# Kernel tuning notes

Measured on AMD Instinct MI355X. Metric: run time of the kernel, lower is better.

## Reference

```python
import jax, jax.numpy as jnp
import numpy as np
import math

D_MODEL = 1024
N_HEADS = 16
D_K = 64
CHUNK_LEN = 64


def setup_inputs() -> dict:
    key = jax.random.key(0)
    ks = jax.random.split(key, 12)
    hd = N_HEADS * D_K
    s = 0.02
    return {
        'h': jax.random.normal(ks[0], (4, 2048, D_MODEL), jnp.float32),
        'e': jax.random.normal(ks[1], (4, 32, 2, 128, D_MODEL), jnp.float32),
        'Wq': jax.random.normal(ks[2], (D_MODEL, hd), jnp.float32) * s,
        'bq': jnp.zeros((hd,), jnp.float32),
        'Wk': jax.random.normal(ks[3], (D_MODEL, hd), jnp.float32) * s,
        'bk': jnp.zeros((hd,), jnp.float32),
        'Wv': jax.random.normal(ks[4], (D_MODEL, hd), jnp.float32) * s,
        'bv': jnp.zeros((hd,), jnp.float32),
        'Wo': jax.random.normal(ks[5], (hd, D_MODEL), jnp.float32) * s,
        'bo': jnp.zeros((D_MODEL,), jnp.float32),
        'gamma': jnp.ones((D_MODEL,), jnp.float32),
        'beta': jnp.zeros((D_MODEL,), jnp.float32),
    }


def reference(h, e, Wq, bq, Wk, bk, Wv, bv, Wo, bo, gamma, beta):
    b, chunks, neighbors, nlen, d_model = e.shape
    seq_len = h.shape[1]
    scale = 1.0 / math.sqrt(D_K)
    h_res = h
    # shift so chunk i attends to neighbors retrieved for chunk i
    hh = h[:, CHUNK_LEN - 1:]
    # layer norm
    mu = jnp.mean(hh, axis=-1, keepdims=True)
    var = jnp.mean(jnp.square(hh - mu), axis=-1, keepdims=True)
    hh = (hh - mu) / jnp.sqrt(var + 1e-5) * gamma + beta
    # pad to chunks * CHUNK_LEN
    pad = chunks * CHUNK_LEN - hh.shape[1]
    hh = jnp.pad(hh, ((0, 0), (0, pad), (0, 0)))
    hh = hh.reshape(b, chunks, CHUNK_LEN, d_model)
    q = (hh @ Wq + bq).reshape(b, chunks, CHUNK_LEN, N_HEADS, D_K)
    k = (e @ Wk + bk).reshape(b, chunks, neighbors, nlen, N_HEADS, D_K)
    v = (e @ Wv + bv).reshape(b, chunks, neighbors, nlen, N_HEADS, D_K)
    attn = jnp.einsum('bcihd,bcnjhd->bchinj', q, k) * scale  # [b,c,h,i,n,j]
    a_shape = attn.shape
    attn = jax.nn.softmax(attn.reshape(*a_shape[:-2], -1), axis=-1).reshape(a_shape)
    out = jnp.einsum('bchinj,bcnjhd->bcihd', attn, v)
    out = out.reshape(b, chunks * CHUNK_LEN, N_HEADS * D_K)
    out = out @ Wo + bo
    out = jnp.pad(out, ((0, 0), (CHUNK_LEN - 1, 0), (0, 0)))
    return out[:, :seq_len] + h_res
```

## Files before the change

kernel.cpp:

```cpp
#include <hip/hip_runtime.h>
#include <cstdint>
#include <cstddef>


typedef float f32x4 __attribute__((ext_vector_type(4)));
typedef __bf16 bf16x8 __attribute__((ext_vector_type(8)));

static __device__ __forceinline__ ushort f2bf(float f) {
  union { float f; uint32_t u; } x; x.f = f;
  uint32_t r = x.u + 0x7fffu + ((x.u >> 16) & 1u);
  return (ushort)(r >> 16);
}

static __device__ __forceinline__ bf16x8 ld_frag(const ushort* p) {
  union { uint4 u; bf16x8 v; } x;
  x.u = *(const uint4*)p;
  return x.v;
}

static __device__ __forceinline__ void gl2lds16(const ushort* g, ushort* l) {
  __builtin_amdgcn_global_load_lds(
      (const __attribute__((address_space(1))) void*)g,
      (__attribute__((address_space(3))) void*)l,
      16, 0, 0);
}

__global__ __launch_bounds__(256) void prep_kernel(const float* __restrict__ Wq,
                                                   const float* __restrict__ Wk,
                                                   const float* __restrict__ Wv,
                                                   const float* __restrict__ Wo,
                                                   const float* __restrict__ h,
                                                   const float* __restrict__ gamma,
                                                   const float* __restrict__ beta,
                                                   ushort* __restrict__ WqT,
                                                   ushort* __restrict__ WkvT,
                                                   ushort* __restrict__ WoT,
                                                   ushort* __restrict__ lnout) {
  __shared__ float tile[64][65];
  __shared__ float a1[4], a2[4];
  const int t = threadIdx.x;
  const int bx = blockIdx.x;

  if (bx < 1024) {
    const int z = bx >> 8, rem = bx & 255;
    const int n0 = (rem & 15) * 64, k0 = (rem >> 4) * 64;
    const float* W; ushort* WT;
    switch (z) {
      case 0:  W = Wq; WT = WqT; break;
      case 1:  W = Wk; WT = WkvT; break;
      case 2:  W = Wv; WT = WkvT + (size_t)1024 * 1024; break;
      default: W = Wo; WT = WoT; break;
    }
#pragma unroll
    for (int i = 0; i < 4; ++i) {
      int lid = i * 256 + t;
      int r = lid >> 4, c4 = (lid & 15) * 4;
      float4 v = *(const float4*)&W[(size_t)(k0 + r) * 1024 + n0 + c4];
      tile[r][c4 + 0] = v.x; tile[r][c4 + 1] = v.y;
      tile[r][c4 + 2] = v.z; tile[r][c4 + 3] = v.w;
    }
    __syncthreads();
#pragma unroll
    for (int i = 0; i < 4; ++i) {
      int lid = i * 256 + t;
      int n = lid >> 4, k4 = (lid & 15) * 4;
      ushort4 o;
      o.x = f2bf(tile[k4 + 0][n]); o.y = f2bf(tile[k4 + 1][n]);
      o.z = f2bf(tile[k4 + 2][n]); o.w = f2bf(tile[k4 + 3][n]);
      *(ushort4*)&WT[(size_t)(n0 + n) * 1024 + k0 + k4] = o;
    }
    return;
  }

  const int bx2 = bx - 1024;
  const int b = bx2 >> 11, s = bx2 & 2047;
  ushort* orow = lnout + (size_t)(b * 2048 + s) * 1024;
  if (s >= 1985) {
    ushort4 z4; z4.x = 0; z4.y = 0; z4.z = 0; z4.w = 0;
    *(ushort4*)&orow[t * 4] = z4;
    return;
  }
  const float* xrow = h + (size_t)(b * 2048 + 63 + s) * 1024;
  float4 x = *(const float4*)&xrow[t * 4];
  float s1 = x.x + x.y + x.z + x.w;
  float s2 = x.x * x.x + x.y * x.y + x.z * x.z + x.w * x.w;
#pragma unroll
  for (int off = 32; off > 0; off >>= 1) {
    s1 += __shfl_xor(s1, off);
    s2 += __shfl_xor(s2, off);
  }
  if ((t & 63) == 0) { a1[t >> 6] = s1; a2[t >> 6] = s2; }
  __syncthreads();
  s1 = a1[0] + a1[1] + a1[2] + a1[3];
  s2 = a2[0] + a2[1] + a2[2] + a2[3];
  const float mu = s1 * (1.0f / 1024.0f);
  const float var = s2 * (1.0f / 1024.0f) - mu * mu;
  const float rstd = rsqrtf(var + 1e-5f);
  float4 g = *(const float4*)&gamma[t * 4];
  float4 be = *(const float4*)&beta[t * 4];
  ushort4 o;
  o.x = f2bf((x.x - mu) * rstd * g.x + be.x);
  o.y = f2bf((x.y - mu) * rstd * g.y + be.y);
  o.z = f2bf((x.z - mu) * rstd * g.z + be.z);
  o.w = f2bf((x.w - mu) * rstd * g.w + be.w);
  *(ushort4*)&orow[t * 4] = o;
}

__global__ __launch_bounds__(256) void cast_bf16(const float* __restrict__ x,
                                                 ushort* __restrict__ y) {
  const size_t i = ((size_t)blockIdx.x * 256 + threadIdx.x) * 8;
  float4 a = *(const float4*)&x[i];
  float4 b = *(const float4*)&x[i + 4];
  ushort o[8];
  o[0] = f2bf(a.x); o[1] = f2bf(a.y); o[2] = f2bf(a.z); o[3] = f2bf(a.w);
  o[4] = f2bf(b.x); o[5] = f2bf(b.y); o[6] = f2bf(b.z); o[7] = f2bf(b.w);
  *(uint4*)&y[i] = *(const uint4*)o;
}

__global__ __launch_bounds__(256) void qproj_cast(const ushort* __restrict__ A,
                                                  const ushort* __restrict__ Bt,
                                                  const float* __restrict__ bias,
                                                  ushort* __restrict__ Cbf,
                                                  float scale,
                                                  const float* __restrict__ ex,
                                                  ushort* __restrict__ ey) {
  if (blockIdx.x >= 512) {
    const size_t i = ((size_t)(blockIdx.x - 512) * 256 + threadIdx.x) * 8;
    float4 a = *(const float4*)&ex[i];
    float4 b = *(const float4*)&ex[i + 4];
    ushort o[8];
    o[0] = f2bf(a.x); o[1] = f2bf(a.y); o[2] = f2bf(a.z); o[3] = f2bf(a.w);
    o[4] = f2bf(b.x); o[5] = f2bf(b.y); o[6] = f2bf(b.z); o[7] = f2bf(b.w);
    *(uint4*)&ey[i] = *(const uint4*)o;
    return;
  }
  __shared__ __align__(16) ushort Alds[2][128 * 32];
  __shared__ __align__(16) ushort Blds[2][128 * 32];
  const int t = threadIdx.x;
  const int lane = t & 63, wave = t >> 6;
  const int quad = lane >> 4, l16 = lane & 15;

  const int L = blockIdx.x;
  const int xcd = L & 7, slot = L >> 3;
  const int nt = slot & 7;
  const int mt = xcd * 8 + (slot >> 3);
  const int m0 = mt * 128, n0 = nt * 128;

  const int srow = lane >> 2;
  const int scol = (lane & 3) * 8;
  const int c0 = wave * 2;
  const ushort* gA0 = A  + (size_t)(m0 + c0 * 16 + srow) * 1024 + scol;
  const ushort* gA1 = gA0 + 16 * 1024;
  const ushort* gB0 = Bt + (size_t)(n0 + c0 * 16 + srow) * 1024 + scol;
  const ushort* gB1 = gB0 + 16 * 1024;
  ushort* dA0 = &Alds[0][c0 * 512 + lane * 8];
  ushort* dA1 = dA0 + 512;
  ushort* dB0 = &Blds[0][c0 * 512 + lane * 8];
  ushort* dB1 = dB0 + 512;
  const ptrdiff_t SUB = 128 * 32;

  const int wrow = (wave >> 1) * 64, wcol = (wave & 1) * 64;
  const ushort* pA = &Alds[0][(wrow + l16) * 32 + quad * 8];
  const ushort* pB = &Blds[0][(wcol + l16) * 32 + quad * 8];

  f32x4 zero = {0.f, 0.f, 0.f, 0.f};
  f32x4 acc[4][4];
#pragma unroll
  for (int i = 0; i < 4; ++i)
#pragma unroll
    for (int j = 0; j < 4; ++j) acc[i][j] = zero;

  for (int kb = 0; kb < 16; ++kb) {
    const int ko = kb * 64;
    gl2lds16(gA0 + ko, dA0);         gl2lds16(gA1 + ko, dA1);
    gl2lds16(gA0 + ko + 32, dA0 + SUB); gl2lds16(gA1 + ko + 32, dA1 + SUB);
    gl2lds16(gB0 + ko, dB0);         gl2lds16(gB1 + ko, dB1);
    gl2lds16(gB0 + ko + 32, dB0 + SUB); gl2lds16(gB1 + ko + 32, dB1 + SUB);
    __syncthreads();
#pragma unroll
    for (int sub = 0; sub < 2; ++sub) {
      bf16x8 af[4], bfv[4];
#pragma unroll
      for (int i = 0; i < 4; ++i) af[i]  = ld_frag(pA + sub * SUB + i * 512);
#pragma unroll
      for (int j = 0; j < 4; ++j) bfv[j] = ld_frag(pB + sub * SUB + j * 512);
#pragma unroll
      for (int i = 0; i < 4; ++i)
#pragma unroll
        for (int j = 0; j < 4; ++j)
          acc[i][j] = __builtin_amdgcn_mfma_f32_16x16x32_bf16(af[i], bfv[j], acc[i][j], 0, 0, 0);
    }
    __syncthreads();
  }

#pragma unroll
  for (int mi = 0; mi < 4; ++mi)
#pragma unroll
    for (int mj = 0; mj < 4; ++mj) {
      const int cc = n0 + wcol + mj * 16 + l16;
      const int r0 = m0 + wrow + mi * 16 + quad * 4;
      const float bvb = bias[cc];
#pragma unroll
      for (int rr = 0; rr < 4; ++rr)
        Cbf[(size_t)(r0 + rr) * 1024 + cc] = f2bf((acc[mi][mj][rr] + bvb) * scale);
    }
}

template <int MODE, int NT>
__global__ __launch_bounds__(256) void gemm_bf16(const ushort* __restrict__ A,
                                                 const ushort* __restrict__ Bt,
                                                 const float* __restrict__ bias,
                                                 float* __restrict__ Cf,
                                                 const float* __restrict__ resid,
                                                 int mtiles) {
  if (blockIdx.x >= 512) {
    const int idx4 = (blockIdx.x - 512) * 256 + threadIdx.x;
    const int b = idx4 / 16128;
    const int rem = idx4 - b * 16128;
    const size_t o = (size_t)b * 2048 * 1024 + (size_t)rem * 4;
    *(float4*)&Cf[o] = *(const float4*)&resid[o];
    return;
  }
  __shared__ __align__(16) ushort Alds[2][128 * 32];
  __shared__ __align__(16) ushort Blds[2][128 * 32];
  const int t = threadIdx.x;
  const int lane = t & 63, wave = t >> 6;
  const int quad = lane >> 4, l16 = lane & 15;

  const int L = blockIdx.x;
  const int xcd = L & 7, slot = L >> 3;
  const int nt = slot & (NT - 1);
  const int mt = xcd * (mtiles >> 3) + (slot / NT);
  const int m0 = mt * 128, n0 = nt * 128;

  const int srow = lane >> 2;
  const int scol = (lane & 3) * 8;
  const int c0 = wave * 2;
  const ushort* gA0 = A  + (size_t)(m0 + c0 * 16 + srow) * 1024 + scol;
  const ushort* gA1 = gA0 + 16 * 1024;
  const ushort* gB0 = Bt + (size_t)(n0 + c0 * 16 + srow) * 1024 + scol;
  const ushort* gB1 = gB0 + 16 * 1024;
  ushort* dA0 = &Alds[0][c0 * 512 + lane * 8];
  ushort* dA1 = dA0 + 512;
  ushort* dB0 = &Blds[0][c0 * 512 + lane * 8];
  ushort* dB1 = dB0 + 512;
  const ptrdiff_t SUB = 128 * 32;

  const int wrow = (wave >> 1) * 64, wcol = (wave & 1) * 64;
  const ushort* pA = &Alds[0][(wrow + l16) * 32 + quad * 8];
  const ushort* pB = &Blds[0][(wcol + l16) * 32 + quad * 8];

  f32x4 zero = {0.f, 0.f, 0.f, 0.f};
  f32x4 acc[4][4];
#pragma unroll
  for (int i = 0; i < 4; ++i)
#pragma unroll
    for (int j = 0; j < 4; ++j) acc[i][j] = zero;

  for (int kb = 0; kb < 16; ++kb) {
    const int ko = kb * 64;
    gl2lds16(gA0 + ko, dA0);         gl2lds16(gA1 + ko, dA1);
    gl2lds16(gA0 + ko + 32, dA0 + SUB); gl2lds16(gA1 + ko + 32, dA1 + SUB);
    gl2lds16(gB0 + ko, dB0);         gl2lds16(gB1 + ko, dB1);
    gl2lds16(gB0 + ko + 32, dB0 + SUB); gl2lds16(gB1 + ko + 32, dB1 + SUB);
    __syncthreads();
#pragma unroll
    for (int sub = 0; sub < 2; ++sub) {
      bf16x8 af[4], bfv[4];
#pragma unroll
      for (int i = 0; i < 4; ++i) af[i]  = ld_frag(pA + sub * SUB + i * 512);
#pragma unroll
      for (int j = 0; j < 4; ++j) bfv[j] = ld_frag(pB + sub * SUB + j * 512);
#pragma unroll
      for (int i = 0; i < 4; ++i)
#pragma unroll
        for (int j = 0; j < 4; ++j)
          acc[i][j] = __builtin_amdgcn_mfma_f32_16x16x32_bf16(af[i], bfv[j], acc[i][j], 0, 0, 0);
    }
    __syncthreads();
  }

#pragma unroll
  for (int mi = 0; mi < 4; ++mi)
#pragma unroll
    for (int mj = 0; mj < 4; ++mj) {
      const int cc = n0 + wcol + mj * 16 + l16;
      const int r0 = m0 + wrow + mi * 16 + quad * 4;
      const float bvb = bias[cc];
#pragma unroll
      for (int rr = 0; rr < 4; ++rr) {
        const int r = r0 + rr;
        const int b = r >> 11, s = r & 2047;
        if (s < 1985) {
          const size_t o = (size_t)(b * 2048 + s + 63) * 1024 + cc;
          Cf[o] = acc[mi][mj][rr] + bvb + resid[o];
        }
      }
    }
}

__global__ __launch_bounds__(512, 2) void gemm_kv256(const ushort* __restrict__ A,
                                                     const ushort* __restrict__ Bt,
                                                     const float* __restrict__ bk_,
                                                     const float* __restrict__ bv_,
                                                     ushort* __restrict__ Kout,
                                                     ushort* __restrict__ Vtg,
                                                     int mrow_off) {
  __shared__ __align__(16) ushort Alds[4 * 8192];
  __shared__ __align__(16) ushort Blds[4 * 8192];

  const int t = threadIdx.x;
  const int lane = t & 63, wave = t >> 6;
  const int wm = wave >> 2, wn = wave & 3;
  const int l16 = lane & 15, quad = lane >> 4;

  const int L = blockIdx.x;
  const int xcd = L & 7, slot = L >> 3;
  const int nt = slot & 7, mt = xcd * 8 + (slot >> 3);
  const int m0 = mt * 256, n0 = nt * 256;

  const int w2 = wave * 2;
  const int srow = lane >> 3;
  const int lanex = (lane & 7) ^ srow;
  const ushort* gA2 = A  + (size_t)(m0 + w2 * 8 + srow) * 1024 + lanex * 8;
  const ushort* gB2 = Bt + (size_t)(n0 + w2 * 8 + srow) * 1024 + lanex * 8;
  ushort* dA2 = Alds + w2 * 512 + lane * 8;
  ushort* dB2 = Blds + w2 * 512 + lane * 8;

  auto stage_a = [&](int ti, int hh) {
    const ushort* g = gA2 + (size_t)hh * 131072 + (size_t)ti * 64;
    ushort* d = dA2 + ((ti & 1) * 2 + hh) * 8192;
    gl2lds16(g, d);
    gl2lds16(g + 8192, d + 512);
  };
  auto stage_b = [&](int ti, int hh) {
    const ushort* g = gB2 + (size_t)hh * 131072 + (size_t)ti * 64;
    ushort* d = dB2 + ((ti & 1) * 2 + hh) * 8192;
    gl2lds16(g, d);
    gl2lds16(g + 8192, d + 512);
  };

  const int b2 = (l16 >> 2) & 1;
  const int qx = (quad ^ (l16 & 3)) << 3;
  const int kof0 = b2 << 5;
  const int kof1 = 32 - kof0;

  f32x4 zero = {0.f, 0.f, 0.f, 0.f};
  f32x4 acc[8][4];
#pragma unroll
  for (int i = 0; i < 8; ++i)
#pragma unroll
    for (int j = 0; j < 4; ++j) acc[i][j] = zero;

  stage_b(0, 0); stage_a(0, 0); stage_b(0, 1); stage_a(0, 1);
  stage_b(1, 0); stage_a(1, 0); stage_b(1, 1);
  asm volatile("s_waitcnt vmcnt(6)" ::: "memory");
  __builtin_amdgcn_s_barrier();

  bf16x8 a[4][2], b01[2][2], b23[2][2];

#pragma unroll 2
  for (int tt = 0; tt < 16; ++tt) {
    const int cur = tt & 1;
    const ushort* pa = Alds + (cur * 2 + wm) * 8192 + l16 * 64 + qx;
    const ushort* pb = Blds + (cur * 2 + (wn >> 1)) * 8192 +
                       ((wn & 1) * 64 + l16) * 64 + qx;

#pragma unroll
    for (int mi = 0; mi < 4; ++mi) {
      a[mi][0] = ld_frag(pa + mi * 1024 + kof0);
      a[mi][1] = ld_frag(pa + mi * 1024 + kof1);
    }
#pragma unroll
    for (int ni = 0; ni < 2; ++ni) {
      b01[ni][0] = ld_frag(pb + ni * 1024 + kof0);
      b01[ni][1] = ld_frag(pb + ni * 1024 + kof1);
    }
    if (tt < 15) stage_a(tt + 1, 1);
    __builtin_amdgcn_s_barrier();
    asm volatile("s_waitcnt lgkmcnt(0)" ::: "memory");
    __builtin_amdgcn_sched_barrier(0);
    __builtin_amdgcn_s_setprio(1);
#pragma unroll
    for (int mi = 0; mi < 4; ++mi)
#pragma unroll
      for (int ni = 0; ni < 2; ++ni) {
        acc[mi][ni] = __builtin_amdgcn_mfma_f32_16x16x32_bf16(a[mi][0], b01[ni][0], acc[mi][ni], 0, 0, 0);
        acc[mi][ni] = __builtin_amdgcn_mfma_f32_16x16x32_bf16(a[mi][1], b01[ni][1], acc[mi][ni], 0, 0, 0);
      }
    __builtin_amdgcn_s_setprio(0);
    __builtin_amdgcn_s_barrier();

#pragma unroll
    for (int ni = 0; ni < 2; ++ni) {
      b23[ni][0] = ld_frag(pb + (ni + 2) * 1024 + kof0);
      b23[ni][1] = ld_frag(pb + (ni + 2) * 1024 + kof1);
    }
    if (tt < 14) stage_b(tt + 2, 0);
    __builtin_amdgcn_s_barrier();
    asm volatile("s_waitcnt lgkmcnt(0)" ::: "memory");
    __builtin_amdgcn_sched_barrier(0);
    __builtin_amdgcn_s_setprio(1);
#pragma unroll
    for (int mi = 0; mi < 4; ++mi)
#pragma unroll
      for (int ni = 0; ni < 2; ++ni) {
        acc[mi][ni + 2] = __builtin_amdgcn_mfma_f32_16x16x32_bf16(a[mi][0], b23[ni][0], acc[mi][ni + 2], 0, 0, 0);
        acc[mi][ni + 2] = __builtin_amdgcn_mfma_f32_16x16x32_bf16(a[mi][1], b23[ni][1], acc[mi][ni + 2], 0, 0, 0);
      }
    __builtin_amdgcn_s_setprio(0);
    __builtin_amdgcn_s_barrier();

#pragma unroll
    for (int mi = 0; mi < 4; ++mi) {
      a[mi][0] = ld_frag(pa + (mi + 4) * 1024 + kof0);
      a[mi][1] = ld_frag(pa + (mi + 4) * 1024 + kof1);
    }
    if (tt < 14) stage_b(tt + 2, 1);
    __builtin_amdgcn_s_barrier();
    asm volatile("s_waitcnt lgkmcnt(0)" ::: "memory");
    __builtin_amdgcn_sched_barrier(0);
    __builtin_amdgcn_s_setprio(1);
#pragma unroll
    for (int mi = 0; mi < 4; ++mi)
#pragma unroll
      for (int ni = 0; ni < 2; ++ni) {
        acc[mi + 4][ni + 2] = __builtin_amdgcn_mfma_f32_16x16x32_bf16(a[mi][0], b23[ni][0], acc[mi + 4][ni + 2], 0, 0, 0);
        acc[mi + 4][ni + 2] = __builtin_amdgcn_mfma_f32_16x16x32_bf16(a[mi][1], b23[ni][1], acc[mi + 4][ni + 2], 0, 0, 0);
      }
    __builtin_amdgcn_s_setprio(0);
    __builtin_amdgcn_s_barrier();

    if (tt < 14) stage_a(tt + 2, 0);
    __builtin_amdgcn_s_barrier();
    __builtin_amdgcn_s_setprio(1);
#pragma unroll
    for (int mi = 0; mi < 4; ++mi)
#pragma unroll
      for (int ni = 0; ni < 2; ++ni) {
        acc[mi + 4][ni] = __builtin_amdgcn_mfma_f32_16x16x32_bf16(a[mi][0], b01[ni][0], acc[mi + 4][ni], 0, 0, 0);
        acc[mi + 4][ni] = __builtin_amdgcn_mfma_f32_16x16x32_bf16(a[mi][1], b01[ni][1], acc[mi + 4][ni], 0, 0, 0);
      }
    __builtin_amdgcn_s_setprio(0);
    if (tt < 15) {
      if (tt == 14) asm volatile("s_waitcnt vmcnt(0)" ::: "memory");
      else          asm volatile("s_waitcnt vmcnt(6)" ::: "memory");
      __builtin_amdgcn_s_barrier();
    }
  }

  const int rbase = m0 + wm * 128 + quad * 4;
  const int cbase = n0 + wn * 64 + l16;
  if (n0 < 1024) {
#pragma unroll
    for (int mi = 0; mi < 8; ++mi)
#pragma unroll
      for (int ni = 0; ni < 4; ++ni) {
        const int cc = cbase + ni * 16;
        const float bb = bk_[cc];
        const int r0 = rbase + mi * 16;
#pragma unroll
        for (int rr = 0; rr < 4; ++rr)
          Kout[(size_t)(r0 + rr) * 1024 + cc] = f2bf(acc[mi][ni][rr] + bb);
      }
  } else {
#pragma unroll
    for (int mi = 0; mi < 8; ++mi)
#pragma unroll
      for (int ni = 0; ni < 4; ++ni) {
        const int cv = cbase - 1024 + ni * 16;
        const int hh_ = cv >> 6, dd = cv & 63;
        const float bb = bv_[cv];
        const int gr0 = rbase + mi * 16 + mrow_off;
        const int bcl = gr0 >> 8, j0 = gr0 & 255;
        ushort4 o;
        o.x = f2bf(acc[mi][ni][0] + bb);
        o.y = f2bf(acc[mi][ni][1] + bb);
        o.z = f2bf(acc[mi][ni][2] + bb);
        o.w = f2bf(acc[mi][ni][3] + bb);
        *(ushort4*)&Vtg[(size_t)(bcl * 16 + hh_) * 16384 + dd * 256 + j0] = o;
      }
  }
}

__global__ __launch_bounds__(256, 2) void attn_kernel(const ushort* __restrict__ Qb,
                                                      const ushort* __restrict__ Kb,
                                                      const ushort* __restrict__ Vtg,
                                                      ushort* __restrict__ Ob) {
  __shared__ __align__(16) ushort Plds[4][4096];

  const int t = threadIdx.x;
  const int lane = t & 63, wave = t >> 6;
  const int quad = lane >> 4, l16 = lane & 15;
  const int hw = blockIdx.x * 4 + wave;
  const int hd = hw & 15, c = (hw >> 4) & 31, b = hw >> 9;

  const int qrow0 = b * 2048 + c * 64;
  const int kvrow0 = (b * 32 + c) * 256;
  const int colh = hd * 64;
  const ushort* vsrc = Vtg + ((size_t)((b * 32 + c) * 16 + hd)) * 16384;
  char* pw = (char*)&Plds[wave][0];
  const int swz = (l16 & 7) << 4;

  bf16x8 qf[4][2];
#pragma unroll
  for (int qq = 0; qq < 4; ++qq)
#pragma unroll
    for (int cc = 0; cc < 2; ++cc)
      qf[qq][cc] = ld_frag(&Qb[(size_t)(qrow0 + qq * 16 + l16) * 1024 +
                               colh + cc * 32 + quad * 8]);

  f32x4 zero = {0.f, 0.f, 0.f, 0.f};
  f32x4 Ot[4][4];
#pragma unroll
  for (int dd = 0; dd < 4; ++dd)
#pragma unroll
    for (int qq = 0; qq < 4; ++qq) Ot[dd][qq] = zero;
  float m[4], l[4];
#pragma unroll
  for (int qq = 0; qq < 4; ++qq) { m[qq] = -1e30f; l[qq] = 0.f; }

  for (int kb = 0; kb < 4; ++kb) {
    bf16x8 kf[4][2];
#pragma unroll
    for (int kk = 0; kk < 4; ++kk)
#pragma unroll
      for (int cc = 0; cc < 2; ++cc)
        kf[kk][cc] = ld_frag(&Kb[(size_t)(kvrow0 + kb * 64 + kk * 16 + l16) * 1024 +
                                 colh + cc * 32 + quad * 8]);

    f32x4 st[4][4];
#pragma unroll
    for (int kk = 0; kk < 4; ++kk)
#pragma unroll
      for (int qq = 0; qq < 4; ++qq) st[kk][qq] = zero;
#pragma unroll
    for (int cc = 0; cc < 2; ++cc)
#pragma unroll
      for (int kk = 0; kk < 4; ++kk)
#pragma unroll
        for (int qq = 0; qq < 4; ++qq)
          st[kk][qq] = __builtin_amdgcn_mfma_f32_16x16x32_bf16(kf[kk][cc], qf[qq][cc], st[kk][qq], 0, 0, 0);

    bf16x8 vf[4][2];
#pragma unroll
    for (int dd = 0; dd < 4; ++dd)
#pragma unroll
      for (int cc = 0; cc < 2; ++cc)
        vf[dd][cc] = ld_frag(&vsrc[(dd * 16 + l16) * 256 + kb * 64 + cc * 32 + quad * 8]);

#pragma unroll
    for (int qq = 0; qq < 4; ++qq) {
      float bm = st[0][qq][0];
#pragma unroll
      for (int kk = 0; kk < 4; ++kk)
#pragma unroll
        for (int rr = 0; rr < 4; ++rr) bm = fmaxf(bm, st[kk][qq][rr]);
      bm = fmaxf(bm, __shfl_xor(bm, 16));
      bm = fmaxf(bm, __shfl_xor(bm, 32));
      const float mn = fmaxf(m[qq], bm);
      const float sc = exp2f(m[qq] - mn);
      float bs = 0.f;
#pragma unroll
      for (int kk = 0; kk < 4; ++kk)
#pragma unroll
        for (int rr = 0; rr < 4; ++rr) {
          float p = exp2f(st[kk][qq][rr] - mn);
          st[kk][qq][rr] = p;
          bs += p;
        }
      bs += __shfl_xor(bs, 16);
      bs += __shfl_xor(bs, 32);
      l[qq] = l[qq] * sc + bs;
      m[qq] = mn;
#pragma unroll
      for (int dd = 0; dd < 4; ++dd) Ot[dd][qq] *= sc;
      const int rowb = (qq * 16 + l16) * 128;
#pragma unroll
      for (int kk = 0; kk < 4; ++kk) {
        uint32_t w0 = (uint32_t)f2bf(st[kk][qq][0]) | ((uint32_t)f2bf(st[kk][qq][1]) << 16);
        uint32_t w1 = (uint32_t)f2bf(st[kk][qq][2]) | ((uint32_t)f2bf(st[kk][qq][3]) << 16);
        const int byte = rowb + ((kk * 32 + quad * 8) ^ swz);
        *(uint32_t*)(pw + byte) = w0;
        *(uint32_t*)(pw + byte + 4) = w1;
      }
    }

#pragma unroll
    for (int qq = 0; qq < 4; ++qq)
#pragma unroll
      for (int cc = 0; cc < 2; ++cc) {
        const int byte = (qq * 16 + l16) * 128 + ((cc * 64 + quad * 16) ^ swz);
        bf16x8 pf = ld_frag((const ushort*)(pw + byte));
#pragma unroll
        for (int dd = 0; dd < 4; ++dd)
          Ot[dd][qq] = __builtin_amdgcn_mfma_f32_16x16x32_bf16(vf[dd][cc], pf, Ot[dd][qq], 0, 0, 0);
      }
  }

#pragma unroll
  for (int qq = 0; qq < 4; ++qq) {
    const float inv = 1.0f / l[qq];
    const int rowb = (qq * 16 + l16) * 128;
#pragma unroll
    for (int dd = 0; dd < 4; ++dd) {
      f32x4 v = Ot[dd][qq];
      uint32_t w0 = (uint32_t)f2bf(v[0] * inv) | ((uint32_t)f2bf(v[1] * inv) << 16);
      uint32_t w1 = (uint32_t)f2bf(v[2] * inv) | ((uint32_t)f2bf(v[3] * inv) << 16);
      const int byte = rowb + ((dd * 32 + quad * 8) ^ swz);
      *(uint32_t*)(pw + byte) = w0;
      *(uint32_t*)(pw + byte + 4) = w1;
    }
  }
#pragma unroll
  for (int p = 0; p < 8; ++p) {
    const int r = p * 8 + (lane >> 3);
    const int ch = lane & 7;
    const int byte = r * 128 + ((ch * 16) ^ ((r & 7) << 4));
    uint4 o = *(const uint4*)(pw + byte);
    *(uint4*)&Ob[(size_t)(qrow0 + r) * 1024 + colh + ch * 8] = o;
  }
}

extern "C" void kernel_launch(void* const* d_in, const int* in_sizes, int n_in,
                              void* d_out, int out_size, void* d_ws, size_t ws_size,
                              hipStream_t stream) {
  const float* h     = (const float*)d_in[0];
  const float* e     = (const float*)d_in[1];
  const float* Wq    = (const float*)d_in[2];
  const float* bq    = (const float*)d_in[3];
  const float* Wk    = (const float*)d_in[4];
  const float* bk    = (const float*)d_in[5];
  const float* Wv    = (const float*)d_in[6];
  const float* bv    = (const float*)d_in[7];
  const float* Wo    = (const float*)d_in[8];
  const float* bo    = (const float*)d_in[9];
  const float* gamma = (const float*)d_in[10];
  const float* beta  = (const float*)d_in[11];
  float* out = (float*)d_out;

  char* ws = (char*)d_ws;
  ushort* stg  = (ushort*)(ws + ((size_t)0 << 20));
  ushort* WqT  = (ushort*)(ws + ((size_t)32 << 20));
  ushort* WkvT = (ushort*)(ws + ((size_t)34 << 20));
  ushort* WoT  = (ushort*)(ws + ((size_t)38 << 20));
  ushort* Qb   = (ushort*)(ws + ((size_t)40 << 20));
  ushort* Kb   = (ushort*)(ws + ((size_t)56 << 20));
  ushort* VtG  = (ushort*)(ws + ((size_t)120 << 20));

  prep_kernel<<<9216, 256, 0, stream>>>(Wq, Wk, Wv, Wo, h, gamma, beta,
                                        WqT, WkvT, WoT, VtG);

  qproj_cast<<<8704, 256, 0, stream>>>(VtG, WqT, bq, Qb,
                                       0.125f * 1.4426950408889634f,
                                       e, stg);

  gemm_kv256<<<512, 512, 0, stream>>>(stg, WkvT, bk, bv, Kb, VtG, 0);
  cast_bf16<<<8192, 256, 0, stream>>>(e + (size_t)16384 * 1024, stg);
  gemm_kv256<<<512, 512, 0, stream>>>(stg, WkvT, bk, bv,
                                      Kb + (size_t)16384 * 1024, VtG, 16384);

  attn_kernel<<<512, 256, 0, stream>>>(Qb, Kb, VtG, stg);

  gemm_bf16<1, 8><<<764, 256, 0, stream>>>(stg, WoT, bo, out, h, 64);
}
```

Before: 498.2 us.

## Split KV projection into quarters and fuse next-quarter e cast into GEMM launches

The K/V projection over the neighbor tensor now runs as four quarter-sized GEMM launches with a double-buffered bf16 staging area. Each launch carries extra blocks that cast the next quarter of e from fp32 to bf16, so the cast overlaps GEMM work and the standalone cast kernel is gone. The output-projection GEMM template is specialised to fixed tile counts. This adds launches and smaller GEMM grids (256 tiles each), which may lower utilisation per launch, and the cast blocks compete with GEMM blocks for bandwidth and compute units.

```diff
diff --git a/kernel.cpp b/kernel.cpp
--- a/kernel.cpp
+++ b/kernel.cpp
@@ -104,17 +104,6 @@
   o.z = f2bf((x.z - mu) * rstd * g.z + be.z);
   o.w = f2bf((x.w - mu) * rstd * g.w + be.w);
   *(ushort4*)&orow[t * 4] = o;
-}
-
-__global__ __launch_bounds__(256) void cast_bf16(const float* __restrict__ x,
-                                                 ushort* __restrict__ y) {
-  const size_t i = ((size_t)blockIdx.x * 256 + threadIdx.x) * 8;
-  float4 a = *(const float4*)&x[i];
-  float4 b = *(const float4*)&x[i + 4];
-  ushort o[8];
-  o[0] = f2bf(a.x); o[1] = f2bf(a.y); o[2] = f2bf(a.z); o[3] = f2bf(a.w);
-  o[4] = f2bf(b.x); o[5] = f2bf(b.y); o[6] = f2bf(b.z); o[7] = f2bf(b.w);
-  *(uint4*)&y[i] = *(const uint4*)o;
 }
 
 __global__ __launch_bounds__(256) void qproj_cast(const ushort* __restrict__ A,
@@ -206,13 +195,11 @@
     }
 }
 
-template <int MODE, int NT>
-__global__ __launch_bounds__(256) void gemm_bf16(const ushort* __restrict__ A,
-                                                 const ushort* __restrict__ Bt,
-                                                 const float* __restrict__ bias,
-                                                 float* __restrict__ Cf,
-                                                 const float* __restrict__ resid,
-                                                 int mtiles) {
+__global__ __launch_bounds__(256) void gemm_oproj(const ushort* __restrict__ A,
+                                                  const ushort* __restrict__ Bt,
+                                                  const float* __restrict__ bias,
+                                                  float* __restrict__ Cf,
+                                                  const float* __restrict__ resid) {
   if (blockIdx.x >= 512) {
     const int idx4 = (blockIdx.x - 512) * 256 + threadIdx.x;
     const int b = idx4 / 16128;
@@ -229,8 +216,8 @@
 
   const int L = blockIdx.x;
   const int xcd = L & 7, slot = L >> 3;
-  const int nt = slot & (NT - 1);
-  const int mt = xcd * (mtiles >> 3) + (slot / NT);
+  const int nt = slot & 7;
+  const int mt = xcd * 8 + (slot >> 3);
   const int m0 = mt * 128, n0 = nt * 128;
 
   const int srow = lane >> 2;
@@ -305,7 +292,20 @@
                                                      const float* __restrict__ bv_,
                                                      ushort* __restrict__ Kout,
                                                      ushort* __restrict__ Vtg,
-                                                     int mrow_off) {
+                                                     int mrow_off,
+                                                     const float* __restrict__ ecast_src,
+                                                     ushort* __restrict__ ecast_dst) {
+  if (blockIdx.x >= 256) {
+    const size_t i = ((size_t)(blockIdx.x - 256) * 512 + threadIdx.x) * 8;
+    float4 a = *(const float4*)&ecast_src[i];
+    float4 b = *(const float4*)&ecast_src[i + 4];
+    ushort o[8];
+    o[0] = f2bf(a.x); o[1] = f2bf(a.y); o[2] = f2bf(a.z); o[3] = f2bf(a.w);
+    o[4] = f2bf(b.x); o[5] = f2bf(b.y); o[6] = f2bf(b.z); o[7] = f2bf(b.w);
+    *(uint4*)&ecast_dst[i] = *(const uint4*)o;
+    return;
+  }
+
   __shared__ __align__(16) ushort Alds[4 * 8192];
   __shared__ __align__(16) ushort Blds[4 * 8192];
 
@@ -316,7 +316,7 @@
 
   const int L = blockIdx.x;
   const int xcd = L & 7, slot = L >> 3;
-  const int nt = slot & 7, mt = xcd * 8 + (slot >> 3);
+  const int nt = slot & 7, mt = xcd * 4 + (slot >> 3);
   const int m0 = mt * 256, n0 = nt * 256;
 
   const int w2 = wave * 2;
@@ -647,20 +647,26 @@
   ushort* Qb   = (ushort*)(ws + ((size_t)40 << 20));
   ushort* Kb   = (ushort*)(ws + ((size_t)56 << 20));
   ushort* VtG  = (ushort*)(ws + ((size_t)120 << 20));
+  const size_t QROWS = 8192;
+  ushort* stgP[2] = { stg, stg + QROWS * 1024 };
 
   prep_kernel<<<9216, 256, 0, stream>>>(Wq, Wk, Wv, Wo, h, gamma, beta,
                                         WqT, WkvT, WoT, VtG);
 
-  qproj_cast<<<8704, 256, 0, stream>>>(VtG, WqT, bq, Qb,
+  qproj_cast<<<4608, 256, 0, stream>>>(VtG, WqT, bq, Qb,
                                        0.125f * 1.4426950408889634f,
-                                       e, stg);
-
-  gemm_kv256<<<512, 512, 0, stream>>>(stg, WkvT, bk, bv, Kb, VtG, 0);
-  cast_bf16<<<8192, 256, 0, stream>>>(e + (size_t)16384 * 1024, stg);
-  gemm_kv256<<<512, 512, 0, stream>>>(stg, WkvT, bk, bv,
-                                      Kb + (size_t)16384 * 1024, VtG, 16384);
+                                       e, stgP[0]);
+
+  for (int q = 0; q < 4; ++q) {
+    const int nblk = (q < 3) ? 2304 : 256;
+    gemm_kv256<<<nblk, 512, 0, stream>>>(stgP[q & 1], WkvT, bk, bv,
+                                         Kb + (size_t)q * QROWS * 1024, VtG,
+                                         q * 8192,
+                                         e + (size_t)(q + 1) * QROWS * 1024,
+                                         stgP[(q + 1) & 1]);
+  }
 
   attn_kernel<<<512, 256, 0, stream>>>(Qb, Kb, VtG, stg);
 
-  gemm_bf16<1, 8><<<764, 256, 0, stream>>>(stg, WoT, bo, out, h, 64);
-}
+  gemm_oproj<<<764, 256, 0, stream>>>(stg, WoT, bo, out, h);
+}
```

Result: slower. 514.5 us (+3.3%).
